# Kernel tuning notes

Hardware: AMD Instinct MI355X
Metric: run time of the kernel (lower is better)

## Reference

```python
import jax, jax.numpy as jnp
import numpy as np

B = 65536

def _conv(x, w, stride=(1, 1), padding='VALID', groups=1):
    return jax.lax.conv_general_dilated(
        x, w, window_strides=stride, padding=padding,
        dimension_numbers=('NCHW', 'OIHW', 'NCHW'), feature_group_count=groups)

def _lstm_step(x, h, c, w_ih, w_hh, b_ih, b_hh):
    # PyTorch gate order: i, f, g, o
    gates = x @ w_ih.T + h @ w_hh.T + b_ih + b_hh
    i, f, g, o = jnp.split(gates, 4, axis=-1)
    c_new = jax.nn.sigmoid(f) * c + jax.nn.sigmoid(i) * jnp.tanh(g)
    h_new = jax.nn.sigmoid(o) * jnp.tanh(c_new)
    return h_new, c_new


def setup_inputs() -> dict:
    key = jax.random.key(0)
    ks = jax.random.split(key, 32)
    s = 0.1
    inp = {
        'x': jax.random.normal(ks[0], (B, 3, 41), jnp.float32),
        'lstm1_h': jax.random.normal(ks[1], (B, 64), jnp.float32),
        'lstm1_b': jax.random.normal(ks[2], (B, 64), jnp.float32),
        'lstm2_h': jax.random.normal(ks[3], (B, 64), jnp.float32),
        'lstm2_b': jax.random.normal(ks[4], (B, 64), jnp.float32),
        # conv stack params
        'conv_dw_w': jax.random.normal(ks[5], (1, 1, 3, 3), jnp.float32) * s,
        'conv_pw_w': jax.random.normal(ks[6], (16, 1, 1, 1), jnp.float32) * s,
        'conv_pw_b': jax.random.normal(ks[7], (16,), jnp.float32) * s,
        'sep1_dw_w': jax.random.normal(ks[8], (16, 1, 1, 3), jnp.float32) * s,
        'sep1_pw_w': jax.random.normal(ks[9], (16, 16, 1, 1), jnp.float32) * s,
        'sep1_pw_b': jax.random.normal(ks[10], (16,), jnp.float32) * s,
        'sep2_dw_w': jax.random.normal(ks[11], (16, 1, 1, 3), jnp.float32) * s,
        'sep2_pw_w': jax.random.normal(ks[12], (16, 16, 1, 1), jnp.float32) * s,
        'sep2_pw_b': jax.random.normal(ks[13], (16,), jnp.float32) * s,
        # lstm1: input 80, hidden 64
        'w_ih1': jax.random.normal(ks[14], (256, 80), jnp.float32) * s,
        'w_hh1': jax.random.normal(ks[15], (256, 64), jnp.float32) * s,
        'b_ih1': jax.random.normal(ks[16], (256,), jnp.float32) * s,
        'b_hh1': jax.random.normal(ks[17], (256,), jnp.float32) * s,
        # lstm2: input 64, hidden 64
        'w_ih2': jax.random.normal(ks[18], (256, 64), jnp.float32) * s,
        'w_hh2': jax.random.normal(ks[19], (256, 64), jnp.float32) * s,
        'b_ih2': jax.random.normal(ks[20], (256,), jnp.float32) * s,
        'b_hh2': jax.random.normal(ks[21], (256,), jnp.float32) * s,
        # fc head
        'fc1_w': jax.random.normal(ks[22], (32, 128), jnp.float32) * s,
        'fc1_b': jax.random.normal(ks[23], (32,), jnp.float32) * s,
        'fc2_w': jax.random.normal(ks[24], (1, 32), jnp.float32) * s,
        'fc2_b': jax.random.normal(ks[25], (1,), jnp.float32) * s,
    }
    return inp


def reference(x, lstm1_h, lstm1_b, lstm2_h, lstm2_b,
              conv_dw_w, conv_pw_w, conv_pw_b,
              sep1_dw_w, sep1_pw_w, sep1_pw_b,
              sep2_dw_w, sep2_pw_w, sep2_pw_b,
              w_ih1, w_hh1, b_ih1, b_hh1,
              w_ih2, w_hh2, b_ih2, b_hh2,
              fc1_w, fc1_b, fc2_w, fc2_b):
    b = x.shape[0]
    y = x.reshape(b, 1, 3, 41)
    y = _conv(y, conv_dw_w)                                   # [B,1,1,39]
    y = _conv(y, conv_pw_w) + conv_pw_b[None, :, None, None]  # [B,16,1,39]
    y = jax.nn.relu(y)
    y = jax.lax.reduce_window(y, -jnp.inf, jax.lax.max,
                              (1, 1, 1, 3), (1, 1, 1, 2), 'VALID')  # [B,16,1,19]
    y = _conv(y, sep1_dw_w, stride=(2, 2), padding=((0, 0), (1, 1)), groups=16)  # [B,16,1,10]
    y = _conv(y, sep1_pw_w) + sep1_pw_b[None, :, None, None]
    y = jax.nn.relu(y)
    y = jnp.pad(y, ((0, 0), (0, 0), (0, 0), (0, 1)))          # [B,16,1,11]
    y = _conv(y, sep2_dw_w, stride=(2, 2), groups=16)         # [B,16,1,5]
    y = _conv(y, sep2_pw_w) + sep2_pw_b[None, :, None, None]
    y = jax.nn.relu(y)
    feat = y[:, :, 0, :].transpose(0, 2, 1).reshape(b, 80)    # permute(0,2,1) then flatten W*C
    h1, c1 = _lstm_step(feat, lstm1_h, lstm1_b, w_ih1, w_hh1, b_ih1, b_hh1)
    h2, c2 = _lstm_step(h1, lstm2_h, lstm2_b, w_ih2, w_hh2, b_ih2, b_hh2)
    z = jnp.concatenate([h2, h1], axis=-1)                    # [B,128]
    z = jax.nn.relu(z @ fc1_w.T + fc1_b)
    prob = jax.nn.sigmoid(z @ fc2_w.T + fc2_b)                # [B,1]
    return (prob[:, None, :], h1[None], c1[None], h2[None], c2[None])
```

## Files before the change

kernel.cpp:

```cpp
#include <hip/hip_runtime.h>

typedef unsigned short u16;
typedef __attribute__((ext_vector_type(8))) _Float16 f16x8;
typedef __attribute__((ext_vector_type(4))) float f32x4;

#define NT 256
#define BT 64
#define CBT 32
#define A1S 152
#define A2S 136

__device__ __forceinline__ u16 f2h(float f) {
  _Float16 h = (_Float16)f;
  union { _Float16 h; u16 u; } c; c.h = h; return c.u;
}
__device__ __forceinline__ float sigm(float x) { return 1.0f / (1.0f + __expf(-x)); }
__device__ __forceinline__ float tanh_(float x) {
  float ax = fabsf(x);
  float e = __expf(-2.0f * ax);
  float t = (1.0f - e) / (1.0f + e);
  return copysignf(t, x);
}
__device__ __forceinline__ uint2 packh4(float4 v) {
  return make_uint2((unsigned)f2h(v.x) | ((unsigned)f2h(v.y) << 16),
                    (unsigned)f2h(v.z) | ((unsigned)f2h(v.w) << 16));
}

#define WS_W1   0
#define WS_W2   40960
#define WS_FC1  73728
#define WS_CW   77824
#define WS_BOFF 159744
#define WS_CF   161792
#define WS_FEAT_U16 81088


__global__ __launch_bounds__(NT) void prep(
    const float* __restrict__ wih1, const float* __restrict__ whh1,
    const float* __restrict__ wih2, const float* __restrict__ whh2,
    const float* __restrict__ fc1w,
    const float* __restrict__ bih1, const float* __restrict__ bhh1,
    const float* __restrict__ bih2, const float* __restrict__ bhh2,
    const float* __restrict__ dwWg, const float* __restrict__ pwWg, const float* __restrict__ pwBg,
    const float* __restrict__ s1dwg, const float* __restrict__ s1pwg, const float* __restrict__ s1pbg,
    const float* __restrict__ s2dwg, const float* __restrict__ s2pwg, const float* __restrict__ s2pbg,
    u16* __restrict__ wbf, float* __restrict__ bc, float* __restrict__ cf)
{
  int i = blockIdx.x * NT + threadIdx.x;
  if (i < 40960) {
    int j8 = i & 7, l = (i >> 3) & 63, rem = i >> 9;
    int kc = rem % 5, gw = rem / 5;
    int n = (gw >> 2) * 64 + (gw & 3) * 16 + (l & 15);
    int k = kc * 32 + (l >> 4) * 8 + j8;
    float v = 0.f;
    if (k < 80) v = wih1[n * 80 + k];
    else if (k < 144) v = whh1[n * 64 + (k - 80)];
    wbf[i] = f2h(v);
  } else if (i < 73728) {
    int t2 = i - 40960;
    int j8 = t2 & 7, l = (t2 >> 3) & 63, rem = t2 >> 9;
    int kc = rem & 3, gw = rem >> 2;
    int n = (gw >> 2) * 64 + (gw & 3) * 16 + (l & 15);
    int k = kc * 32 + (l >> 4) * 8 + j8;
    float v = (k < 64) ? wih2[n * 64 + k] : whh2[n * 64 + (k - 64)];
    wbf[i] = f2h(v);
  } else if (i < 77824) {
    int t2 = i - 73728;
    int j8 = t2 & 7, l = (t2 >> 3) & 63, rem = t2 >> 9;
    int kc = rem & 3, nt = rem >> 2;
    int n = nt * 16 + (l & 15);
    int k = kc * 32 + (l >> 4) * 8 + j8;
    int ks = (k < 64) ? k + 64 : k - 64;
    wbf[i] = f2h(fc1w[n * 128 + ks]);
  } else if (i < 79872) {
    int t2 = i - 77824;
    int frag = t2 >> 9, u = t2 & 511;
    int j8 = u & 7, l = (u >> 3) & 63;
    int co = l & 15, kk = (l >> 4) * 8 + j8;
    float v = 0.f;
    if (frag == 0) { int k = kk >> 4, ci = kk & 15; v = s1dwg[ci * 3 + k] * s1pwg[co * 16 + ci]; }
    else if (frag == 1) { if (kk < 16) v = s1dwg[kk * 3 + 2] * s1pwg[co * 16 + kk]; }
    else if (frag == 2) { int k = kk >> 4, ci = kk & 15; v = s2dwg[ci * 3 + k] * s2pwg[co * 16 + ci]; }
    else { if (kk < 16) v = s2dwg[kk * 3 + 2] * s2pwg[co * 16 + kk]; }
    wbf[i] = f2h(v);
  }
  if (i < 256)      bc[i] = bih1[i] + bhh1[i];
  else if (i < 512) bc[i] = bih2[i - 256] + bhh2[i - 256];
  if (i < 89) {
    float v;
    if (i < 16)      { float w = pwWg[i];      v = w > 0.f ? w : 0.f; }
    else if (i < 32) { float w = pwWg[i - 16]; v = w > 0.f ? 0.f : w; }
    else if (i < 48) v = pwBg[i - 32];
    else if (i < 64) v = s1pbg[i - 48];
    else if (i < 80) v = s2pbg[i - 64];
    else             v = dwWg[i - 80];
    cf[i] = v;
  }
}

#define CV_CW   0
#define CV_Y0   384
#define CV_XS   5504
#define CV_P    5504
#define CV_U1   27008
#define CV_FL   384
#define CV_SIZE 38272

__global__ __launch_bounds__(NT, 4) void convk(
    const float* __restrict__ xg, const u16* __restrict__ wbf,
    const float* __restrict__ cf, u16* __restrict__ featg)
{
  __shared__ __align__(16) unsigned char smem[CV_SIZE];
  const int t = threadIdx.x;
  const int blk = blockIdx.x;
  const int base = blk * CBT;

  float* cw = (float*)(smem + CV_CW);
  float* y0 = (float*)(smem + CV_Y0);
  float* xs = (float*)(smem + CV_XS);
  u16* pp  = (u16*)(smem + CV_P);
  u16* u1  = (u16*)(smem + CV_U1);
  u16* fl  = (u16*)(smem + CV_FL);

  const int lane = t & 63, wv = t >> 6, l15 = lane & 15, q16 = lane >> 4;

  const u16* Wf = wbf + WS_CW;
  f16x8 W1a = *(const f16x8*)(Wf + lane * 8);
  f16x8 W1b = *(const f16x8*)(Wf + 512 + lane * 8);
  f16x8 W2a = *(const f16x8*)(Wf + 1024 + lane * 8);
  f16x8 W2b = *(const f16x8*)(Wf + 1536 + lane * 8);

  if (t < 96) cw[t] = (t < 89) ? cf[t] : 0.f;
  {
    const float4* src = (const float4*)xg + (size_t)blk * 984;
    for (int i = t; i < 984; i += NT) *(float4*)(xs + i * 4) = src[i];
  }
  if (t < 64) {
    uint4 z; z.x = z.y = z.z = z.w = 0u;
    *(uint4*)(u1 + ((t >> 1) * 11 + 10) * 16 + (t & 1) * 8) = z;
  }
  __syncthreads();

  {
    float d0 = cw[80], d1 = cw[81], d2 = cw[82], d3 = cw[83], d4 = cw[84],
          d5 = cw[85], d6 = cw[86], d7 = cw[87], d8 = cw[88];
    int b = t >> 3, w0 = (t & 7) * 5;
    const float* xb = xs + b * 123;
    float* yb = y0 + b * 40;
#pragma unroll
    for (int s = 0; s < 5; ++s) {
      int w = w0 + s;
      if (w < 39) {
        float v = d0 * xb[w]      + d1 * xb[w + 1]  + d2 * xb[w + 2]
                + d3 * xb[41 + w] + d4 * xb[42 + w] + d5 * xb[43 + w]
                + d6 * xb[82 + w] + d7 * xb[83 + w] + d8 * xb[84 + w];
        yb[w] = v;
      }
    }
  }
  __syncthreads();

  {
    uint4 z; z.x = z.y = z.z = z.w = 0u;
    if (t < 128) {
      int b = t >> 2, sub = t & 3;
      int col = (sub >> 1) ? 20 : 0;
      *(uint4*)(pp + (b * 21 + col) * 16 + (sub & 1) * 8) = z;
    }
    int b = t >> 3, u = t & 7, half = u >> 2, w5b = u & 3;
    float ph[8], pl[8], pb[8];
    ((float4*)ph)[0] = *(float4*)(cw + half * 8);
    ((float4*)ph)[1] = *(float4*)(cw + half * 8 + 4);
    ((float4*)pl)[0] = *(float4*)(cw + 16 + half * 8);
    ((float4*)pl)[1] = *(float4*)(cw + 16 + half * 8 + 4);
    ((float4*)pb)[0] = *(float4*)(cw + 32 + half * 8);
    ((float4*)pb)[1] = *(float4*)(cw + 32 + half * 8 + 4);
    const float* yb = y0 + b * 40;
#pragma unroll
    for (int s = 0; s < 5; ++s) {
      int w5 = w5b + s * 4;
      if (w5 < 19) {
        float a0 = yb[2 * w5], a1 = yb[2 * w5 + 1], a2 = yb[2 * w5 + 2];
        float mx = fmaxf(a0, fmaxf(a1, a2));
        float mn = fminf(a0, fminf(a1, a2));
        unsigned pk[4];
#pragma unroll
        for (int c = 0; c < 4; ++c) {
          float v0 = fmaxf(fmaf(ph[2 * c],     mx, fmaf(pl[2 * c],     mn, pb[2 * c])),     0.f);
          float v1 = fmaxf(fmaf(ph[2 * c + 1], mx, fmaf(pl[2 * c + 1], mn, pb[2 * c + 1])), 0.f);
          pk[c] = (unsigned)f2h(v0) | ((unsigned)f2h(v1) << 16);
        }
        uint4 st; st.x = pk[0]; st.y = pk[1]; st.z = pk[2]; st.w = pk[3];
        *(uint4*)(pp + (b * 21 + w5 + 1) * 16 + half * 8) = st;
      }
    }
  }
  __syncthreads();

  {
    float sb1 = cw[48 + l15];
    int kA = q16 >> 1, ciA = (q16 & 1) * 8;
#pragma unroll
    for (int s = 0; s < 5; ++s) {
      int tile = wv + s * 4;
      int rowA = tile * 16 + l15;
      int bA = rowA / 10, qA = rowA - bA * 10;
      f16x8 a0 = *(const f16x8*)(pp + (bA * 21 + 2 * qA + kA) * 16 + ciA);
      f16x8 a1 = *(const f16x8*)(pp + (bA * 21 + 2 * qA + 2) * 16 + ciA);
      f32x4 acc = {0.f, 0.f, 0.f, 0.f};
      acc = __builtin_amdgcn_mfma_f32_16x16x32_f16(a0, W1a, acc, 0, 0, 0);
      acc = __builtin_amdgcn_mfma_f32_16x16x32_f16(a1, W1b, acc, 0, 0, 0);
#pragma unroll
      for (int r = 0; r < 4; ++r) {
        int rowg = tile * 16 + q16 * 4 + r;
        int bC = rowg / 10, qC = rowg - bC * 10;
        u1[(bC * 11 + qC) * 16 + l15] = f2h(fmaxf(acc[r] + sb1, 0.f));
      }
    }
  }
  __syncthreads();

  {
    float sb2 = cw[64 + l15];
    int kA = q16 >> 1, ciA = (q16 & 1) * 8;
    for (int tile = wv; tile < 10; tile += 4) {
      int rowA = tile * 16 + l15;
      int bA = rowA / 5, rA = rowA - bA * 5;
      f16x8 a0 = *(const f16x8*)(u1 + (bA * 11 + 2 * rA + kA) * 16 + ciA);
      f16x8 a1 = *(const f16x8*)(u1 + (bA * 11 + 2 * rA + 2) * 16 + ciA);
      f32x4 acc = {0.f, 0.f, 0.f, 0.f};
      acc = __builtin_amdgcn_mfma_f32_16x16x32_f16(a0, W2a, acc, 0, 0, 0);
      acc = __builtin_amdgcn_mfma_f32_16x16x32_f16(a1, W2b, acc, 0, 0, 0);
#pragma unroll
      for (int r = 0; r < 4; ++r) {
        int rowg = tile * 16 + q16 * 4 + r;
        int bC = rowg / 5, rC = rowg - bC * 5;
        fl[bC * 80 + rC * 16 + l15] = f2h(fmaxf(acc[r] + sb2, 0.f));
      }
    }
  }
  __syncthreads();

  {
    const uint4* s4 = (const uint4*)fl;
    uint4* d4 = (uint4*)(featg + (size_t)base * 80);
    for (int i = t; i < 320; i += NT) d4[i] = s4[i];
  }
}

#define LO_B1   0
#define LO_B2   256
#define LO_FC1B 512
#define LO_FC2W 544
#define LO_FC2B 576
#define LR_A1 2560
#define LR_A2 22080
#define LSMEM 39488

__global__ __launch_bounds__(NT, 3) void lstmk(
    const float* __restrict__ h1g, const float* __restrict__ c1g,
    const float* __restrict__ h2g, const float* __restrict__ c2g,
    const float* __restrict__ fc1bg, const float* __restrict__ fc2wg, const float* __restrict__ fc2bg,
    const u16* __restrict__ wbf, const float* __restrict__ bc, const u16* __restrict__ featg,
    float* __restrict__ out, int B)
{
  __shared__ __align__(16) unsigned char smem[LSMEM];
  const int t = threadIdx.x;
  const int blk = blockIdx.x;
  const int base = blk * BT;

  float* sw = (float*)smem;
  u16* A1 = (u16*)(smem + LR_A1);
  float* zz = (float*)(smem + LR_A1);
  u16* A2 = (u16*)(smem + LR_A2);

  float* probO = out;
  float* h1o = out + B;
  float* c1o = out + B + B * 64;
  float* h2o = out + B + B * 128;
  float* c2o = out + B + B * 192;

  const u16* w1f = wbf + WS_W1;
  const u16* w2f = wbf + WS_W2;
  const u16* wFf = wbf + WS_FC1;

  const int w = t >> 6, lane = t & 63, q = lane >> 4, l15 = lane & 15;
  const int j = w * 16 + l15;

  float c1r[16];
#pragma unroll
  for (int mt = 0; mt < 4; ++mt)
#pragma unroll
    for (int r = 0; r < 4; ++r)
      c1r[mt * 4 + r] = c1g[(size_t)(base + mt * 16 + q * 4 + r) * 64 + j];

  for (int i = t; i < 512; i += NT) sw[i] = bc[i];
  for (int i = t; i < 32;  i += NT) sw[LO_FC1B + i] = fc1bg[i];
  for (int i = t; i < 32;  i += NT) sw[LO_FC2W + i] = fc2wg[i];
  if (t == 0) sw[LO_FC2B] = fc2bg[0];
  for (int i = t; i < 640; i += NT) {
    int m = i / 10, o = (i - m * 10) * 8;
    *(uint4*)(A1 + m * A1S + o) = *(const uint4*)(featg + (size_t)(base + m) * 80 + o);
  }
  {
    const float4* hsrc = (const float4*)h1g + (size_t)blk * 1024;
    for (int i = t; i < 1024; i += NT) {
      int m = i >> 4, j4 = (i & 15) * 4;
      *(uint2*)(A1 + m * A1S + 80 + j4) = packh4(hsrc[i]);
    }
  }
  for (int i = t; i < 64; i += NT) {
    uint4 z; z.x = z.y = z.z = z.w = 0u;
    *(uint4*)(A1 + i * A1S + 144) = z;
  }
  if (t == 0) {
    uint4 z; z.x = z.y = z.z = z.w = 0u;
    *(uint4*)(A1 + 64 * A1S) = z;
  }
  {
    const float4* hsrc = (const float4*)h2g + (size_t)blk * 1024;
    for (int i = t; i < 1024; i += NT) {
      int m = i >> 4, j4 = (i & 15) * 4;
      *(uint2*)(A2 + m * A2S + 64 + j4) = packh4(hsrc[i]);
    }
  }
  __syncthreads();

  float c2r[16];

  {
    f16x8 bf1[4][5];
#pragma unroll
    for (int g = 0; g < 4; ++g)
#pragma unroll
      for (int kc = 0; kc < 5; ++kc)
        bf1[g][kc] = *(const f16x8*)(w1f + (size_t)((((g * 4 + w) * 5 + kc) * 64) + lane) * 8);
    float bI = sw[LO_B1 + j], bF = sw[LO_B1 + 64 + j], bG = sw[LO_B1 + 128 + j], bO = sw[LO_B1 + 192 + j];

#pragma unroll 1
    for (int mt = 0; mt < 4; ++mt) {
      f32x4 acc[4];
#pragma unroll
      for (int g = 0; g < 4; ++g) { acc[g][0] = 0.f; acc[g][1] = 0.f; acc[g][2] = 0.f; acc[g][3] = 0.f; }
      const u16* aB = A1 + (mt * 16 + l15) * A1S + q * 8;
#pragma unroll
      for (int kc = 0; kc < 5; ++kc) {
        f16x8 af = *(const f16x8*)(aB + kc * 32);
#pragma unroll
        for (int g = 0; g < 4; ++g)
          acc[g] = __builtin_amdgcn_mfma_f32_16x16x32_f16(af, bf1[g][kc], acc[g], 0, 0, 0);
      }
#pragma unroll
      for (int r = 0; r < 4; ++r) {
        int m = mt * 16 + q * 4 + r;
        int b = base + m;
        float iv = acc[0][r] + bI;
        float fv = acc[1][r] + bF;
        float gv = acc[2][r] + bG;
        float ov = acc[3][r] + bO;
        float cn = sigm(fv) * c1r[mt * 4 + r] + sigm(iv) * tanh_(gv);
        float hn = sigm(ov) * tanh_(cn);
        c1o[b * 64 + j] = cn;
        h1o[b * 64 + j] = hn;
        A2[m * A2S + j] = f2h(hn);
      }
    }
#pragma unroll
    for (int mt = 0; mt < 4; ++mt)
#pragma unroll
      for (int r = 0; r < 4; ++r)
        c2r[mt * 4 + r] = c2g[(size_t)(base + mt * 16 + q * 4 + r) * 64 + j];
  }
  __syncthreads();

  {
    f16x8 bf2[4][4];
#pragma unroll
    for (int g = 0; g < 4; ++g)
#pragma unroll
      for (int kc = 0; kc < 4; ++kc)
        bf2[g][kc] = *(const f16x8*)(w2f + (size_t)((((g * 4 + w) * 4 + kc) * 64) + lane) * 8);
    float bI = sw[LO_B2 + j], bF = sw[LO_B2 + 64 + j], bG = sw[LO_B2 + 128 + j], bO = sw[LO_B2 + 192 + j];

#pragma unroll 1
    for (int mt = 0; mt < 4; ++mt) {
      f32x4 acc[4];
#pragma unroll
      for (int g = 0; g < 4; ++g) { acc[g][0] = 0.f; acc[g][1] = 0.f; acc[g][2] = 0.f; acc[g][3] = 0.f; }
      const u16* aB = A2 + (mt * 16 + l15) * A2S + q * 8;
#pragma unroll
      for (int kc = 0; kc < 4; ++kc) {
        f16x8 af = *(const f16x8*)(aB + kc * 32);
#pragma unroll
        for (int g = 0; g < 4; ++g)
          acc[g] = __builtin_amdgcn_mfma_f32_16x16x32_f16(af, bf2[g][kc], acc[g], 0, 0, 0);
      }
#pragma unroll
      for (int r = 0; r < 4; ++r) {
        int m = mt * 16 + q * 4 + r;
        int b = base + m;
        float iv = acc[0][r] + bI;
        float fv = acc[1][r] + bF;
        float gv = acc[2][r] + bG;
        float ov = acc[3][r] + bO;
        float cn = sigm(fv) * c2r[mt * 4 + r] + sigm(iv) * tanh_(gv);
        float hn = sigm(ov) * tanh_(cn);
        c2o[b * 64 + j] = cn;
        h2o[b * 64 + j] = hn;
        A1[m * A1S + j] = f2h(hn);
      }
    }
  }
  __syncthreads();

  {
    f32x4 accf[2];
#pragma unroll
    for (int nt = 0; nt < 2; ++nt) { accf[nt][0] = 0.f; accf[nt][1] = 0.f; accf[nt][2] = 0.f; accf[nt][3] = 0.f; }
    int m0 = w * 16;
#pragma unroll
    for (int kc = 0; kc < 4; ++kc) {
      f16x8 a = (kc < 2)
        ? *(const f16x8*)(A2 + (m0 + l15) * A2S + kc * 32 + q * 8)
        : *(const f16x8*)(A1 + (m0 + l15) * A1S + (kc - 2) * 32 + q * 8);
#pragma unroll
      for (int nt = 0; nt < 2; ++nt) {
        f16x8 bfr = *(const f16x8*)(wFf + (size_t)(((nt * 4 + kc) * 64) + lane) * 8);
        accf[nt] = __builtin_amdgcn_mfma_f32_16x16x32_f16(a, bfr, accf[nt], 0, 0, 0);
      }
    }
    __syncthreads();
#pragma unroll
    for (int nt = 0; nt < 2; ++nt) {
      int n = nt * 16 + l15;
#pragma unroll
      for (int r = 0; r < 4; ++r) {
        int m = m0 + q * 4 + r;
        zz[m * 33 + n] = fmaxf(accf[nt][r] + sw[LO_FC1B + n], 0.f);
      }
    }
  }
  __syncthreads();

  if (t < 64) {
    int m = t;
    float s = sw[LO_FC2B];
#pragma unroll
    for (int k = 0; k < 32; ++k) s = fmaf(zz[m * 33 + k], sw[LO_FC2W + k], s);
    probO[base + m] = sigm(s);
  }
}

extern "C" void kernel_launch(void* const* d_in, const int* in_sizes, int n_in,
                              void* d_out, int out_size, void* d_ws, size_t ws_size,
                              hipStream_t stream) {
  (void)n_in; (void)out_size; (void)ws_size;
  int B = in_sizes[0] / 123;
  u16* wbf = (u16*)d_ws;
  float* bcm = (float*)((char*)d_ws + WS_BOFF);
  float* cfm = (float*)((char*)d_ws + WS_CF);
  u16* featg = (u16*)d_ws + WS_FEAT_U16;

  hipLaunchKernelGGL(prep, dim3(312), dim3(NT), 0, stream,
      (const float*)d_in[14], (const float*)d_in[15],
      (const float*)d_in[18], (const float*)d_in[19],
      (const float*)d_in[22],
      (const float*)d_in[16], (const float*)d_in[17],
      (const float*)d_in[20], (const float*)d_in[21],
      (const float*)d_in[5], (const float*)d_in[6], (const float*)d_in[7],
      (const float*)d_in[8], (const float*)d_in[9], (const float*)d_in[10],
      (const float*)d_in[11], (const float*)d_in[12], (const float*)d_in[13],
      wbf, bcm, cfm);

  hipLaunchKernelGGL(convk, dim3(B / CBT), dim3(NT), 0, stream,
      (const float*)d_in[0], wbf, cfm, featg);

  hipLaunchKernelGGL(lstmk, dim3(B / BT), dim3(NT), 0, stream,
      (const float*)d_in[1], (const float*)d_in[2],
      (const float*)d_in[3], (const float*)d_in[4],
      (const float*)d_in[23], (const float*)d_in[24], (const float*)d_in[25],
      wbf, bcm, featg,
      (float*)d_out, B);
}
```

Measured before the change: 248.1 us.

## Shrink shared memory in conv and LSTM kernels, replace fc2 LDS reduction with shuffles

The conv kernel now holds the first pointwise-conv accumulators in registers across a barrier so u1 can alias the pooled buffer. That cuts LDS per block and raises launch bounds to 5 blocks. The LSTM kernel drops the separate A2 buffer: h2 input is prefetched into registers, written into A1 after layer 1, and h1 goes to a smaller H1N buffer. This shrinks LDS, and fc2 becomes a wave-shuffle reduction in place of an LDS round trip plus a 64-thread serial loop. Barriers use a custom wait-only-LDS barrier, with extra barriers added and more register pressure as trade-offs.

```diff
diff --git a/kernel.cpp b/kernel.cpp
--- a/kernel.cpp
+++ b/kernel.cpp
@@ -8,7 +8,7 @@
 #define BT 64
 #define CBT 32
 #define A1S 152
-#define A2S 136
+#define H1S 72
 
 __device__ __forceinline__ u16 f2h(float f) {
   _Float16 h = (_Float16)f;
@@ -24,6 +24,11 @@
 __device__ __forceinline__ uint2 packh4(float4 v) {
   return make_uint2((unsigned)f2h(v.x) | ((unsigned)f2h(v.y) << 16),
                     (unsigned)f2h(v.z) | ((unsigned)f2h(v.w) << 16));
+}
+__device__ __forceinline__ void bar() {
+  asm volatile("s_waitcnt lgkmcnt(0)" ::: "memory");
+  __builtin_amdgcn_s_barrier();
+  asm volatile("" ::: "memory");
 }
 
 #define WS_W1   0
@@ -102,11 +107,11 @@
 #define CV_Y0   384
 #define CV_XS   5504
 #define CV_P    5504
-#define CV_U1   27008
+#define CV_U1   5504
 #define CV_FL   384
-#define CV_SIZE 38272
-
-__global__ __launch_bounds__(NT, 4) void convk(
+#define CV_SIZE 27008
+
+__global__ __launch_bounds__(NT, 5) void convk(
     const float* __restrict__ xg, const u16* __restrict__ wbf,
     const float* __restrict__ cf, u16* __restrict__ featg)
 {
@@ -135,11 +140,7 @@
     const float4* src = (const float4*)xg + (size_t)blk * 984;
     for (int i = t; i < 984; i += NT) *(float4*)(xs + i * 4) = src[i];
   }
-  if (t < 64) {
-    uint4 z; z.x = z.y = z.z = z.w = 0u;
-    *(uint4*)(u1 + ((t >> 1) * 11 + 10) * 16 + (t & 1) * 8) = z;
-  }
-  __syncthreads();
+  bar();
 
   {
     float d0 = cw[80], d1 = cw[81], d2 = cw[82], d3 = cw[83], d4 = cw[84],
@@ -158,7 +159,7 @@
       }
     }
   }
-  __syncthreads();
+  bar();
 
   {
     uint4 z; z.x = z.y = z.z = z.w = 0u;
@@ -195,10 +196,10 @@
       }
     }
   }
-  __syncthreads();
-
-  {
-    float sb1 = cw[48 + l15];
+  bar();
+
+  f32x4 acc5[5];
+  {
     int kA = q16 >> 1, ciA = (q16 & 1) * 8;
 #pragma unroll
     for (int s = 0; s < 5; ++s) {
@@ -210,15 +211,28 @@
       f32x4 acc = {0.f, 0.f, 0.f, 0.f};
       acc = __builtin_amdgcn_mfma_f32_16x16x32_f16(a0, W1a, acc, 0, 0, 0);
       acc = __builtin_amdgcn_mfma_f32_16x16x32_f16(a1, W1b, acc, 0, 0, 0);
+      acc5[s] = acc;
+    }
+  }
+  bar();
+  {
+    if (t < 64) {
+      uint4 z; z.x = z.y = z.z = z.w = 0u;
+      *(uint4*)(u1 + ((t >> 1) * 11 + 10) * 16 + (t & 1) * 8) = z;
+    }
+    float sb1 = cw[48 + l15];
+#pragma unroll
+    for (int s = 0; s < 5; ++s) {
+      int tile = wv + s * 4;
 #pragma unroll
       for (int r = 0; r < 4; ++r) {
         int rowg = tile * 16 + q16 * 4 + r;
         int bC = rowg / 10, qC = rowg - bC * 10;
-        u1[(bC * 11 + qC) * 16 + l15] = f2h(fmaxf(acc[r] + sb1, 0.f));
-      }
-    }
-  }
-  __syncthreads();
+        u1[(bC * 11 + qC) * 16 + l15] = f2h(fmaxf(acc5[s][r] + sb1, 0.f));
+      }
+    }
+  }
+  bar();
 
   {
     float sb2 = cw[64 + l15];
@@ -239,7 +253,7 @@
       }
     }
   }
-  __syncthreads();
+  bar();
 
   {
     const uint4* s4 = (const uint4*)fl;
@@ -253,9 +267,9 @@
 #define LO_FC1B 512
 #define LO_FC2W 544
 #define LO_FC2B 576
-#define LR_A1 2560
-#define LR_A2 22080
-#define LSMEM 39488
+#define LR_A1  2560
+#define LR_H1N 22048
+#define LSMEM  31264
 
 __global__ __launch_bounds__(NT, 3) void lstmk(
     const float* __restrict__ h1g, const float* __restrict__ c1g,
@@ -270,9 +284,8 @@
   const int base = blk * BT;
 
   float* sw = (float*)smem;
-  u16* A1 = (u16*)(smem + LR_A1);
-  float* zz = (float*)(smem + LR_A1);
-  u16* A2 = (u16*)(smem + LR_A2);
+  u16* A1  = (u16*)(smem + LR_A1);
+  u16* H1N = (u16*)(smem + LR_H1N);
 
   float* probO = out;
   float* h1o = out + B;
@@ -293,6 +306,13 @@
 #pragma unroll
     for (int r = 0; r < 4; ++r)
       c1r[mt * 4 + r] = c1g[(size_t)(base + mt * 16 + q * 4 + r) * 64 + j];
+
+  uint2 h2p[4];
+  {
+    const float4* hsrc = (const float4*)h2g + (size_t)blk * 1024;
+#pragma unroll
+    for (int k = 0; k < 4; ++k) h2p[k] = packh4(hsrc[t + k * 256]);
+  }
 
   for (int i = t; i < 512; i += NT) sw[i] = bc[i];
   for (int i = t; i < 32;  i += NT) sw[LO_FC1B + i] = fc1bg[i];
@@ -317,14 +337,7 @@
     uint4 z; z.x = z.y = z.z = z.w = 0u;
     *(uint4*)(A1 + 64 * A1S) = z;
   }
-  {
-    const float4* hsrc = (const float4*)h2g + (size_t)blk * 1024;
-    for (int i = t; i < 1024; i += NT) {
-      int m = i >> 4, j4 = (i & 15) * 4;
-      *(uint2*)(A2 + m * A2S + 64 + j4) = packh4(hsrc[i]);
-    }
-  }
-  __syncthreads();
+  bar();
 
   float c2r[16];
 
@@ -362,7 +375,7 @@
         float hn = sigm(ov) * tanh_(cn);
         c1o[b * 64 + j] = cn;
         h1o[b * 64 + j] = hn;
-        A2[m * A2S + j] = f2h(hn);
+        H1N[m * H1S + j] = f2h(hn);
       }
     }
 #pragma unroll
@@ -371,7 +384,16 @@
       for (int r = 0; r < 4; ++r)
         c2r[mt * 4 + r] = c2g[(size_t)(base + mt * 16 + q * 4 + r) * 64 + j];
   }
-  __syncthreads();
+  bar();
+
+  {
+#pragma unroll
+    for (int k = 0; k < 4; ++k) {
+      int i = t + k * 256, m = i >> 4, j4 = (i & 15) * 4;
+      *(uint2*)(A1 + m * A1S + 80 + j4) = h2p[k];
+    }
+  }
+  bar();
 
   {
     f16x8 bf2[4][4];
@@ -387,10 +409,12 @@
       f32x4 acc[4];
 #pragma unroll
       for (int g = 0; g < 4; ++g) { acc[g][0] = 0.f; acc[g][1] = 0.f; acc[g][2] = 0.f; acc[g][3] = 0.f; }
-      const u16* aB = A2 + (mt * 16 + l15) * A2S + q * 8;
+      const u16* aB1 = H1N + (mt * 16 + l15) * H1S + q * 8;
+      const u16* aB2 = A1 + (mt * 16 + l15) * A1S + 80 + q * 8;
 #pragma unroll
       for (int kc = 0; kc < 4; ++kc) {
-        f16x8 af = *(const f16x8*)(aB + kc * 32);
+        f16x8 af = (kc < 2) ? *(const f16x8*)(aB1 + kc * 32)
+                            : *(const f16x8*)(aB2 + (kc - 2) * 32);
 #pragma unroll
         for (int g = 0; g < 4; ++g)
           acc[g] = __builtin_amdgcn_mfma_f32_16x16x32_f16(af, bf2[g][kc], acc[g], 0, 0, 0);
@@ -411,7 +435,7 @@
       }
     }
   }
-  __syncthreads();
+  bar();
 
   {
     f32x4 accf[2];
@@ -421,7 +445,7 @@
 #pragma unroll
     for (int kc = 0; kc < 4; ++kc) {
       f16x8 a = (kc < 2)
-        ? *(const f16x8*)(A2 + (m0 + l15) * A2S + kc * 32 + q * 8)
+        ? *(const f16x8*)(H1N + (m0 + l15) * H1S + kc * 32 + q * 8)
         : *(const f16x8*)(A1 + (m0 + l15) * A1S + (kc - 2) * 32 + q * 8);
 #pragma unroll
       for (int nt = 0; nt < 2; ++nt) {
@@ -429,25 +453,20 @@
         accf[nt] = __builtin_amdgcn_mfma_f32_16x16x32_f16(a, bfr, accf[nt], 0, 0, 0);
       }
     }
-    __syncthreads();
-#pragma unroll
-    for (int nt = 0; nt < 2; ++nt) {
-      int n = nt * 16 + l15;
-#pragma unroll
-      for (int r = 0; r < 4; ++r) {
-        int m = m0 + q * 4 + r;
-        zz[m * 33 + n] = fmaxf(accf[nt][r] + sw[LO_FC1B + n], 0.f);
-      }
-    }
-  }
-  __syncthreads();
-
-  if (t < 64) {
-    int m = t;
-    float s = sw[LO_FC2B];
-#pragma unroll
-    for (int k = 0; k < 32; ++k) s = fmaf(zz[m * 33 + k], sw[LO_FC2W + k], s);
-    probO[base + m] = sigm(s);
+    float fw0 = sw[LO_FC2W + l15], fw1 = sw[LO_FC2W + 16 + l15];
+    float fb0 = sw[LO_FC1B + l15], fb1 = sw[LO_FC1B + 16 + l15];
+    float f2b = sw[LO_FC2B];
+#pragma unroll
+    for (int r = 0; r < 4; ++r) {
+      float zv0 = fmaxf(accf[0][r] + fb0, 0.f);
+      float zv1 = fmaxf(accf[1][r] + fb1, 0.f);
+      float part = fmaf(zv0, fw0, zv1 * fw1);
+      part += __shfl_xor(part, 1);
+      part += __shfl_xor(part, 2);
+      part += __shfl_xor(part, 4);
+      part += __shfl_xor(part, 8);
+      if (l15 == 0) probO[base + m0 + q * 4 + r] = sigm(part + f2b);
+    }
   }
 }
 
```

Result: no change. 247.2 us (-0.3%).
